# Optimization experiments

Measured on AMD Instinct MI355X. Metric: run time of the kernel, lower is better.

## Reference

```python
import jax, jax.numpy as jnp
import numpy as np

B, D, H, W, C = 2, 128, 128, 128, 4
OD, OH, OW = 96, 96, 96
RANK = 3


def setup_inputs() -> dict:
    key = jax.random.key(0)
    k1, k2 = jax.random.split(key)
    inputs = jax.random.normal(k1, (B, D, H, W, C), dtype=jnp.float32)
    # continuous sample coords in [0, size-1] per spatial dim
    scale = jnp.array([D - 1, H - 1, W - 1], dtype=jnp.float32)
    sample_coords = jax.random.uniform(k2, (B, OD, OH, OW, RANK), dtype=jnp.float32) * scale
    return {"inputs": inputs, "sample_coords": sample_coords}


def _pyramid_combination(samples, w_0, w_1):
    # recursive weighted blend over 2^rank corner samples (matches TF module)
    if len(w_0) == 1:
        return samples[0] * w_1[0] + samples[1] * w_0[0]
    f_0 = _pyramid_combination(samples[::2], w_0[:-1], w_1[:-1])
    f_1 = _pyramid_combination(samples[1::2], w_0[:-1], w_1[:-1])
    return f_0 * w_1[-1] + f_1 * w_0[-1]


def reference(inputs, sample_coords):
    # inputs: [B, D, H, W, C]; sample_coords: [B, od, oh, ow, 3]
    in_spatial = inputs.shape[1:-1]
    rank = len(in_spatial)
    batch = inputs.shape[0]

    coords = [sample_coords[..., d] for d in range(rank)]          # each [B, od, oh, ow]
    base = [jnp.floor(c) for c in coords]
    # ZERO boundary -> replicate clamp of integer coords
    floor_i = [jnp.clip(b.astype(jnp.int32), 0, in_spatial[d] - 1) for d, b in enumerate(base)]
    ceil_i = [jnp.clip((b + 1.0).astype(jnp.int32), 0, in_spatial[d] - 1) for d, b in enumerate(base)]

    # ZERO-boundary weights use the CLAMPED corner coords (faithful to source)
    w_0 = [(c - f.astype(jnp.float32))[..., None] for c, f in zip(coords, floor_i)]
    w_1 = [(ce.astype(jnp.float32) - c)[..., None] for c, ce in zip(coords, ceil_i)]

    bids = jnp.arange(batch)[:, None, None, None]                  # broadcast batch ids
    sc = (floor_i, ceil_i)

    samples = []
    for i in range(2 ** rank):
        bits = [(i >> (rank - 1 - d)) & 1 for d in range(rank)]    # dim-0 is most significant bit
        idx = [sc[bits[d]][d] for d in range(rank)]
        samples.append(inputs[bids, idx[0], idx[1], idx[2]])       # [B, od, oh, ow, C]

    return _pyramid_combination(samples, w_0, w_1)
```

## Files before the change

### kernel.cpp

```cpp
#include <hip/hip_runtime.h>


constexpr int D = 128, H = 128, W = 128;
constexpr int OD = 96, OH = 96, OW = 96;
constexpr int VOX_PER_B = OD * OH * OW;
constexpr int NVOX = 2 * VOX_PER_B;

constexpr int NBINS = 1024;
constexpr int NB1 = 216;
constexpr int SPB = 8192;
constexpr int GATHER_THREADS = 1024;
constexpr int TILE_ELEMS = 9 * 5 * 128;

constexpr size_t OFF_MATRIX  = 0;
constexpr size_t OFF_NCNT    = (size_t)NB1 * NBINS * 4;
constexpr size_t OFF_BASE    = OFF_NCNT + NBINS * 4;
constexpr size_t OFF_RECORDS = OFF_BASE + NBINS * 4;
constexpr size_t WS_REQUIRED = OFF_RECORDS + (size_t)NVOX * 16;

__device__ __forceinline__ int bin_of(float cz, float cy, int b) {
    int z0 = min(max((int)floorf(cz), 0), D - 1);
    int y0 = min(max((int)floorf(cy), 0), H - 1);
    return (((b << 4) | (z0 >> 3)) << 5) | (y0 >> 2);
}

__device__ __forceinline__ float4 f4_fma(float w, float4 a, float4 acc) {
    acc.x = fmaf(w, a.x, acc.x);
    acc.y = fmaf(w, a.y, acc.y);
    acc.z = fmaf(w, a.z, acc.z);
    acc.w = fmaf(w, a.w, acc.w);
    return acc;
}
__device__ __forceinline__ float4 f4_scale(float w, float4 a) {
    return make_float4(w * a.x, w * a.y, w * a.z, w * a.w);
}

__global__ __launch_bounds__(1024) void hist_kernel(const float* __restrict__ coords,
                                                    unsigned* __restrict__ matrix) {
    __shared__ unsigned cnt[NBINS];
    const int t = threadIdx.x;
    cnt[t] = 0;
    __syncthreads();
    const int s0 = blockIdx.x * SPB;
#pragma unroll
    for (int j = 0; j < 8; j++) {
        const int s = s0 + j * 1024 + t;
        const float cz = coords[s * 3 + 0];
        const float cy = coords[s * 3 + 1];
        const int b = (s >= VOX_PER_B) ? 1 : 0;
        atomicAdd(&cnt[bin_of(cz, cy, b)], 1u);
    }
    __syncthreads();
    matrix[blockIdx.x * NBINS + t] = cnt[t];
}

__global__ __launch_bounds__(256) void scanA_kernel(unsigned* __restrict__ matrix,
                                                    unsigned* __restrict__ ncnt) {
    const int k = blockIdx.x;
    const int t = threadIdx.x;
    const unsigned v = (t < NB1) ? matrix[t * NBINS + k] : 0u;
    __shared__ unsigned s[256];
    s[t] = v;
    __syncthreads();
    for (int off = 1; off < 256; off <<= 1) {
        unsigned u = (t >= off) ? s[t - off] : 0u;
        __syncthreads();
        s[t] += u;
        __syncthreads();
    }
    if (t < NB1) matrix[t * NBINS + k] = s[t] - v;
    if (t == 255) ncnt[k] = s[255];
}

__global__ __launch_bounds__(1024) void scanB_kernel(const unsigned* __restrict__ ncnt,
                                                     unsigned* __restrict__ base) {
    const int t = threadIdx.x;
    const unsigned v = ncnt[t];
    __shared__ unsigned s[NBINS];
    s[t] = v;
    __syncthreads();
    for (int off = 1; off < NBINS; off <<= 1) {
        unsigned u = (t >= off) ? s[t - off] : 0u;
        __syncthreads();
        s[t] += u;
        __syncthreads();
    }
    base[t] = s[t] - v;
}

__global__ __launch_bounds__(1024) void scatter_kernel(const float* __restrict__ coords,
                                                       const unsigned* __restrict__ matrix,
                                                       const unsigned* __restrict__ base,
                                                       float4* __restrict__ records) {
    __shared__ float4 rec[SPB];
    __shared__ unsigned short binid[SPB];
    __shared__ unsigned cnt[NBINS];
    __shared__ unsigned pref[NBINS];
    __shared__ unsigned gb[NBINS];
    const int t = threadIdx.x;
    const int blk = blockIdx.x;
    cnt[t] = 0;
    gb[t] = base[t] + matrix[blk * NBINS + t];
    __syncthreads();

    const int s0 = blk * SPB;
    float czr[8], cyr[8], cxr[8];
    unsigned rankr[8];
#pragma unroll
    for (int j = 0; j < 8; j++) {
        const int s = s0 + j * 1024 + t;
        czr[j] = coords[s * 3 + 0];
        cyr[j] = coords[s * 3 + 1];
        cxr[j] = coords[s * 3 + 2];
        const int b = (s >= VOX_PER_B) ? 1 : 0;
        rankr[j] = atomicAdd(&cnt[bin_of(czr[j], cyr[j], b)], 1u);
    }
    __syncthreads();

    pref[t] = cnt[t];
    __syncthreads();
    for (int off = 1; off < NBINS; off <<= 1) {
        unsigned u = (t >= off) ? pref[t - off] : 0u;
        __syncthreads();
        pref[t] += u;
        __syncthreads();
    }
    {
        unsigned ex = pref[t] - cnt[t];
        __syncthreads();
        pref[t] = ex;
    }
    __syncthreads();

#pragma unroll
    for (int j = 0; j < 8; j++) {
        const int s = s0 + j * 1024 + t;
        const int b = (s >= VOX_PER_B) ? 1 : 0;
        const int k = bin_of(czr[j], cyr[j], b);
        const unsigned slot = pref[k] + rankr[j];
        rec[slot] = make_float4(czr[j], cyr[j], cxr[j], __uint_as_float((unsigned)s));
        binid[slot] = (unsigned short)k;
    }
    __syncthreads();

#pragma unroll
    for (int j = 0; j < 8; j++) {
        const int i = j * 1024 + t;
        const int k = binid[i];
        records[gb[k] + (unsigned)(i - (int)pref[k])] = rec[i];
    }
}

__global__ __launch_bounds__(GATHER_THREADS) void gather_kernel(
    const float* __restrict__ inp,
    const float4* __restrict__ records,
    const unsigned* __restrict__ base,
    const unsigned* __restrict__ ncnt,
    float4* __restrict__ out)
{
    __shared__ float4 tile[TILE_ELEMS];
    const int k = ((blockIdx.x & 7) << 7) | (blockIdx.x >> 3);
    const int b  = k >> 9;
    const int zb = (k >> 5) & 15;
    const int yb = k & 31;
    const int t = threadIdx.x;

    const float4* bp = (const float4*)inp + ((size_t)b << 21);
    const int zlim = min(9, D - zb * 8);
    const int ylim = min(5, H - yb * 4);
    for (int i = t; i < TILE_ELEMS; i += GATHER_THREADS) {
        const int z = i / 640;
        const int r = i - z * 640;
        const int y = r >> 7;
        const int x = r & 127;
        if (z < zlim && y < ylim)
            tile[i] = bp[((zb * 8 + z) << 14) | ((yb * 4 + y) << 7) | x];
    }
    __syncthreads();

    const unsigned s = base[k];
    const unsigned n = ncnt[k];
    const int zoff = zb * 8, yoff = yb * 4;
    for (unsigned i = s + t; i < s + n; i += GATHER_THREADS) {
        const float4 r = records[i];
        const float cz = r.x, cy = r.y, cx = r.z;
        const unsigned idx = __float_as_uint(r.w);

        const int fz = (int)floorf(cz);
        const int fy = (int)floorf(cy);
        const int fx = (int)floorf(cx);
        const int z1 = min(max(fz + 1, 0), D - 1);
        const int y1 = min(max(fy + 1, 0), H - 1);
        const int x1 = min(max(fx + 1, 0), W - 1);
        const int z0 = min(max(fz, 0), D - 1);
        const int y0 = min(max(fy, 0), H - 1);
        const int x0 = min(max(fx, 0), W - 1);

        const float wz0 = (float)z1 - cz, wz1 = cz - (float)z0;
        const float wy0 = (float)y1 - cy, wy1 = cy - (float)y0;
        const float wx0 = (float)x1 - cx, wx1 = cx - (float)x0;

        const int lz0 = (z0 - zoff) * 640, lz1 = (z1 - zoff) * 640;
        const int ly0 = (y0 - yoff) * 128, ly1 = (y1 - yoff) * 128;

        const float4 s000 = tile[lz0 + ly0 + x0];
        const float4 s001 = tile[lz0 + ly0 + x1];
        const float4 s010 = tile[lz0 + ly1 + x0];
        const float4 s011 = tile[lz0 + ly1 + x1];
        const float4 s100 = tile[lz1 + ly0 + x0];
        const float4 s101 = tile[lz1 + ly0 + x1];
        const float4 s110 = tile[lz1 + ly1 + x0];
        const float4 s111 = tile[lz1 + ly1 + x1];

        float4 c00 = f4_fma(wx1, s001, f4_scale(wx0, s000));
        float4 c01 = f4_fma(wx1, s011, f4_scale(wx0, s010));
        float4 c10 = f4_fma(wx1, s101, f4_scale(wx0, s100));
        float4 c11 = f4_fma(wx1, s111, f4_scale(wx0, s110));
        float4 c0 = f4_fma(wy1, c01, f4_scale(wy0, c00));
        float4 c1 = f4_fma(wy1, c11, f4_scale(wy0, c10));
        out[idx] = f4_fma(wz1, c1, f4_scale(wz0, c0));
    }
}

__global__ __launch_bounds__(256) void direct_kernel(const float* __restrict__ inp,
                                                     const float* __restrict__ coords,
                                                     float4* __restrict__ out) {
    const int idx = blockIdx.x * 256 + threadIdx.x;
    if (idx >= NVOX) return;
    const float cz = coords[idx * 3 + 0];
    const float cy = coords[idx * 3 + 1];
    const float cx = coords[idx * 3 + 2];
    const int b = (idx >= VOX_PER_B) ? 1 : 0;

    const int fz = (int)floorf(cz);
    const int fy = (int)floorf(cy);
    const int fx = (int)floorf(cx);
    const int z1 = min(max(fz + 1, 0), D - 1);
    const int y1 = min(max(fy + 1, 0), H - 1);
    const int x1 = min(max(fx + 1, 0), W - 1);
    const int z0 = min(max(fz, 0), D - 1);
    const int y0 = min(max(fy, 0), H - 1);
    const int x0 = min(max(fx, 0), W - 1);
    const float wz0 = (float)z1 - cz, wz1 = cz - (float)z0;
    const float wy0 = (float)y1 - cy, wy1 = cy - (float)y0;
    const float wx0 = (float)x1 - cx, wx1 = cx - (float)x0;
    const float4* bp = (const float4*)inp + ((size_t)b << 21);
    const int z0o = z0 << 14, z1o = z1 << 14;
    const int y0o = y0 << 7,  y1o = y1 << 7;
    const float4 s000 = bp[z0o | y0o | x0];
    const float4 s001 = bp[z0o | y0o | x1];
    const float4 s010 = bp[z0o | y1o | x0];
    const float4 s011 = bp[z0o | y1o | x1];
    const float4 s100 = bp[z1o | y0o | x0];
    const float4 s101 = bp[z1o | y0o | x1];
    const float4 s110 = bp[z1o | y1o | x0];
    const float4 s111 = bp[z1o | y1o | x1];
    float4 c00 = f4_fma(wx1, s001, f4_scale(wx0, s000));
    float4 c01 = f4_fma(wx1, s011, f4_scale(wx0, s010));
    float4 c10 = f4_fma(wx1, s101, f4_scale(wx0, s100));
    float4 c11 = f4_fma(wx1, s111, f4_scale(wx0, s110));
    float4 c0 = f4_fma(wy1, c01, f4_scale(wy0, c00));
    float4 c1 = f4_fma(wy1, c11, f4_scale(wy0, c10));
    out[idx] = f4_fma(wz1, c1, f4_scale(wz0, c0));
}

extern "C" void kernel_launch(void* const* d_in, const int* in_sizes, int n_in,
                              void* d_out, int out_size, void* d_ws, size_t ws_size,
                              hipStream_t stream) {
    const float* inp    = (const float*)d_in[0];
    const float* coords = (const float*)d_in[1];
    float4* out = (float4*)d_out;

    if (ws_size < WS_REQUIRED) {
        direct_kernel<<<(NVOX + 255) / 256, 256, 0, stream>>>(inp, coords, out);
        return;
    }

    char* ws = (char*)d_ws;
    unsigned* matrix  = (unsigned*)(ws + OFF_MATRIX);
    unsigned* ncnt    = (unsigned*)(ws + OFF_NCNT);
    unsigned* base    = (unsigned*)(ws + OFF_BASE);
    float4*   records = (float4*)(ws + OFF_RECORDS);

    hist_kernel   <<<NB1, 1024, 0, stream>>>(coords, matrix);
    scanA_kernel  <<<NBINS, 256, 0, stream>>>(matrix, ncnt);
    scanB_kernel  <<<1, NBINS, 0, stream>>>(ncnt, base);
    scatter_kernel<<<NB1, 1024, 0, stream>>>(coords, matrix, base, records);
    gather_kernel <<<NBINS, GATHER_THREADS, 0, stream>>>(inp, records, base, ncnt, out);
}
```

Before: 174.5 us.

## Split bins along x, halve gather tiles, pack histogram counts to 16-bit

Adds an x split to the binning (2048 bins instead of 1024), so each gather block stages a 9x5x65 tile, roughly half the previous LDS footprint, and runs with 512 threads. The smaller tile is meant to allow more resident blocks per CU and more overlap between tile loads and gathers. The per-block histogram matrix is stored as packed 16-bit counts to cut workspace traffic, and scatter recomputes bin ids instead of keeping a shared binid array. The cost is more tile halo redundancy along x, more bin-index arithmetic, and a 16-bit limit on the per-block counts.

```diff
diff --git a/kernel.cpp b/kernel.cpp
--- a/kernel.cpp
+++ b/kernel.cpp
@@ -6,22 +6,23 @@
 constexpr int VOX_PER_B = OD * OH * OW;
 constexpr int NVOX = 2 * VOX_PER_B;
 
-constexpr int NBINS = 1024;
+constexpr int NBINS = 2048;
 constexpr int NB1 = 216;
 constexpr int SPB = 8192;
-constexpr int GATHER_THREADS = 1024;
-constexpr int TILE_ELEMS = 9 * 5 * 128;
+constexpr int GT = 512;
+constexpr int TILE_ELEMS = 9 * 5 * 65;
 
 constexpr size_t OFF_MATRIX  = 0;
-constexpr size_t OFF_NCNT    = (size_t)NB1 * NBINS * 4;
+constexpr size_t OFF_NCNT    = 884736;
 constexpr size_t OFF_BASE    = OFF_NCNT + NBINS * 4;
 constexpr size_t OFF_RECORDS = OFF_BASE + NBINS * 4;
 constexpr size_t WS_REQUIRED = OFF_RECORDS + (size_t)NVOX * 16;
 
-__device__ __forceinline__ int bin_of(float cz, float cy, int b) {
+__device__ __forceinline__ int bin_of(float cz, float cy, float cx, int b) {
     int z0 = min(max((int)floorf(cz), 0), D - 1);
     int y0 = min(max((int)floorf(cy), 0), H - 1);
-    return (((b << 4) | (z0 >> 3)) << 5) | (y0 >> 2);
+    int x0 = min(max((int)floorf(cx), 0), W - 1);
+    return (b << 10) | ((z0 >> 3) << 6) | ((y0 >> 2) << 1) | (x0 >> 6);
 }
 
 __device__ __forceinline__ float4 f4_fma(float w, float4 a, float4 acc) {
@@ -36,10 +37,11 @@
 }
 
 __global__ __launch_bounds__(1024) void hist_kernel(const float* __restrict__ coords,
-                                                    unsigned* __restrict__ matrix) {
+                                                    unsigned* __restrict__ matrix32) {
     __shared__ unsigned cnt[NBINS];
     const int t = threadIdx.x;
     cnt[t] = 0;
+    cnt[t + 1024] = 0;
     __syncthreads();
     const int s0 = blockIdx.x * SPB;
 #pragma unroll
@@ -47,18 +49,19 @@
         const int s = s0 + j * 1024 + t;
         const float cz = coords[s * 3 + 0];
         const float cy = coords[s * 3 + 1];
+        const float cx = coords[s * 3 + 2];
         const int b = (s >= VOX_PER_B) ? 1 : 0;
-        atomicAdd(&cnt[bin_of(cz, cy, b)], 1u);
-    }
-    __syncthreads();
-    matrix[blockIdx.x * NBINS + t] = cnt[t];
-}
-
-__global__ __launch_bounds__(256) void scanA_kernel(unsigned* __restrict__ matrix,
+        atomicAdd(&cnt[bin_of(cz, cy, cx, b)], 1u);
+    }
+    __syncthreads();
+    matrix32[blockIdx.x * 1024 + t] = cnt[2 * t] | (cnt[2 * t + 1] << 16);
+}
+
+__global__ __launch_bounds__(256) void scanA_kernel(unsigned short* __restrict__ matrix16,
                                                     unsigned* __restrict__ ncnt) {
     const int k = blockIdx.x;
     const int t = threadIdx.x;
-    const unsigned v = (t < NB1) ? matrix[t * NBINS + k] : 0u;
+    const unsigned v = (t < NB1) ? (unsigned)matrix16[t * NBINS + k] : 0u;
     __shared__ unsigned s[256];
     s[t] = v;
     __syncthreads();
@@ -68,39 +71,41 @@
         s[t] += u;
         __syncthreads();
     }
-    if (t < NB1) matrix[t * NBINS + k] = s[t] - v;
+    if (t < NB1) matrix16[t * NBINS + k] = (unsigned short)(s[t] - v);
     if (t == 255) ncnt[k] = s[255];
 }
 
 __global__ __launch_bounds__(1024) void scanB_kernel(const unsigned* __restrict__ ncnt,
                                                      unsigned* __restrict__ base) {
     const int t = threadIdx.x;
-    const unsigned v = ncnt[t];
-    __shared__ unsigned s[NBINS];
-    s[t] = v;
-    __syncthreads();
-    for (int off = 1; off < NBINS; off <<= 1) {
+    const unsigned c0 = ncnt[2 * t];
+    const unsigned c1 = ncnt[2 * t + 1];
+    __shared__ unsigned s[1024];
+    s[t] = c0 + c1;
+    __syncthreads();
+    for (int off = 1; off < 1024; off <<= 1) {
         unsigned u = (t >= off) ? s[t - off] : 0u;
         __syncthreads();
         s[t] += u;
         __syncthreads();
     }
-    base[t] = s[t] - v;
+    const unsigned ex = s[t] - (c0 + c1);
+    base[2 * t] = ex;
+    base[2 * t + 1] = ex + c0;
 }
 
 __global__ __launch_bounds__(1024) void scatter_kernel(const float* __restrict__ coords,
-                                                       const unsigned* __restrict__ matrix,
+                                                       const unsigned* __restrict__ matrix32,
                                                        const unsigned* __restrict__ base,
                                                        float4* __restrict__ records) {
     __shared__ float4 rec[SPB];
-    __shared__ unsigned short binid[SPB];
-    __shared__ unsigned cnt[NBINS];
+    __shared__ unsigned cntgb[NBINS];
     __shared__ unsigned pref[NBINS];
-    __shared__ unsigned gb[NBINS];
+    __shared__ unsigned s[1024];
     const int t = threadIdx.x;
     const int blk = blockIdx.x;
-    cnt[t] = 0;
-    gb[t] = base[t] + matrix[blk * NBINS + t];
+    cntgb[2 * t] = 0;
+    cntgb[2 * t + 1] = 0;
     __syncthreads();
 
     const int s0 = blk * SPB;
@@ -108,50 +113,56 @@
     unsigned rankr[8];
 #pragma unroll
     for (int j = 0; j < 8; j++) {
-        const int s = s0 + j * 1024 + t;
-        czr[j] = coords[s * 3 + 0];
-        cyr[j] = coords[s * 3 + 1];
-        cxr[j] = coords[s * 3 + 2];
-        const int b = (s >= VOX_PER_B) ? 1 : 0;
-        rankr[j] = atomicAdd(&cnt[bin_of(czr[j], cyr[j], b)], 1u);
-    }
-    __syncthreads();
-
-    pref[t] = cnt[t];
-    __syncthreads();
-    for (int off = 1; off < NBINS; off <<= 1) {
-        unsigned u = (t >= off) ? pref[t - off] : 0u;
-        __syncthreads();
-        pref[t] += u;
-        __syncthreads();
-    }
-    {
-        unsigned ex = pref[t] - cnt[t];
-        __syncthreads();
-        pref[t] = ex;
-    }
+        const int smp = s0 + j * 1024 + t;
+        czr[j] = coords[smp * 3 + 0];
+        cyr[j] = coords[smp * 3 + 1];
+        cxr[j] = coords[smp * 3 + 2];
+        const int b = (smp >= VOX_PER_B) ? 1 : 0;
+        rankr[j] = atomicAdd(&cntgb[bin_of(czr[j], cyr[j], cxr[j], b)], 1u);
+    }
+    __syncthreads();
+
+    const unsigned c0 = cntgb[2 * t];
+    const unsigned c1 = cntgb[2 * t + 1];
+    s[t] = c0 + c1;
+    __syncthreads();
+    for (int off = 1; off < 1024; off <<= 1) {
+        unsigned u = (t >= off) ? s[t - off] : 0u;
+        __syncthreads();
+        s[t] += u;
+        __syncthreads();
+    }
+    const unsigned ex = s[t] - (c0 + c1);
+    pref[2 * t] = ex;
+    pref[2 * t + 1] = ex + c0;
     __syncthreads();
 
 #pragma unroll
     for (int j = 0; j < 8; j++) {
-        const int s = s0 + j * 1024 + t;
-        const int b = (s >= VOX_PER_B) ? 1 : 0;
-        const int k = bin_of(czr[j], cyr[j], b);
-        const unsigned slot = pref[k] + rankr[j];
-        rec[slot] = make_float4(czr[j], cyr[j], cxr[j], __uint_as_float((unsigned)s));
-        binid[slot] = (unsigned short)k;
-    }
+        const int smp = s0 + j * 1024 + t;
+        const int b = (smp >= VOX_PER_B) ? 1 : 0;
+        const int k = bin_of(czr[j], cyr[j], cxr[j], b);
+        rec[pref[k] + rankr[j]] =
+            make_float4(czr[j], cyr[j], cxr[j], __uint_as_float((unsigned)smp));
+    }
+
+    const unsigned m = matrix32[blk * 1024 + t];
+    cntgb[2 * t]     = base[2 * t]     + (m & 0xFFFFu);
+    cntgb[2 * t + 1] = base[2 * t + 1] + (m >> 16);
     __syncthreads();
 
 #pragma unroll
     for (int j = 0; j < 8; j++) {
         const int i = j * 1024 + t;
-        const int k = binid[i];
-        records[gb[k] + (unsigned)(i - (int)pref[k])] = rec[i];
-    }
-}
-
-__global__ __launch_bounds__(GATHER_THREADS) void gather_kernel(
+        const float4 r = rec[i];
+        const unsigned idx = __float_as_uint(r.w);
+        const int b = (idx >= (unsigned)VOX_PER_B) ? 1 : 0;
+        const int k = bin_of(r.x, r.y, r.z, b);
+        records[cntgb[k] + (unsigned)(i - (int)pref[k])] = r;
+    }
+}
+
+__global__ __launch_bounds__(GT) void gather_kernel(
     const float* __restrict__ inp,
     const float4* __restrict__ records,
     const unsigned* __restrict__ base,
@@ -159,29 +170,32 @@
     float4* __restrict__ out)
 {
     __shared__ float4 tile[TILE_ELEMS];
-    const int k = ((blockIdx.x & 7) << 7) | (blockIdx.x >> 3);
-    const int b  = k >> 9;
-    const int zb = (k >> 5) & 15;
-    const int yb = k & 31;
+    const int k = ((blockIdx.x & 7) << 8) | (blockIdx.x >> 3);
+    const int b  = k >> 10;
+    const int zb = (k >> 6) & 15;
+    const int yb = (k >> 1) & 31;
+    const int xb = k & 1;
     const int t = threadIdx.x;
 
     const float4* bp = (const float4*)inp + ((size_t)b << 21);
     const int zlim = min(9, D - zb * 8);
     const int ylim = min(5, H - yb * 4);
-    for (int i = t; i < TILE_ELEMS; i += GATHER_THREADS) {
-        const int z = i / 640;
-        const int r = i - z * 640;
-        const int y = r >> 7;
-        const int x = r & 127;
-        if (z < zlim && y < ylim)
-            tile[i] = bp[((zb * 8 + z) << 14) | ((yb * 4 + y) << 7) | x];
-    }
-    __syncthreads();
-
-    const unsigned s = base[k];
+    for (int i = t; i < TILE_ELEMS; i += GT) {
+        const int z = i / 325;
+        const int r = i - z * 325;
+        const int y = r / 65;
+        const int x = r - y * 65;
+        if (z < zlim && y < ylim) {
+            const int gx = min(xb * 64 + x, W - 1);
+            tile[i] = bp[((zb * 8 + z) << 14) | ((yb * 4 + y) << 7) | gx];
+        }
+    }
+    __syncthreads();
+
+    const unsigned st = base[k];
     const unsigned n = ncnt[k];
-    const int zoff = zb * 8, yoff = yb * 4;
-    for (unsigned i = s + t; i < s + n; i += GATHER_THREADS) {
+    const int zoff = zb * 8, yoff = yb * 4, xoff = xb * 64;
+    for (unsigned i = st + t; i < st + n; i += GT) {
         const float4 r = records[i];
         const float cz = r.x, cy = r.y, cx = r.z;
         const unsigned idx = __float_as_uint(r.w);
@@ -200,17 +214,18 @@
         const float wy0 = (float)y1 - cy, wy1 = cy - (float)y0;
         const float wx0 = (float)x1 - cx, wx1 = cx - (float)x0;
 
-        const int lz0 = (z0 - zoff) * 640, lz1 = (z1 - zoff) * 640;
-        const int ly0 = (y0 - yoff) * 128, ly1 = (y1 - yoff) * 128;
-
-        const float4 s000 = tile[lz0 + ly0 + x0];
-        const float4 s001 = tile[lz0 + ly0 + x1];
-        const float4 s010 = tile[lz0 + ly1 + x0];
-        const float4 s011 = tile[lz0 + ly1 + x1];
-        const float4 s100 = tile[lz1 + ly0 + x0];
-        const float4 s101 = tile[lz1 + ly0 + x1];
-        const float4 s110 = tile[lz1 + ly1 + x0];
-        const float4 s111 = tile[lz1 + ly1 + x1];
+        const int lz0 = (z0 - zoff) * 325, lz1 = (z1 - zoff) * 325;
+        const int ly0 = (y0 - yoff) * 65,  ly1 = (y1 - yoff) * 65;
+        const int lx0 = x0 - xoff,         lx1 = x1 - xoff;
+
+        const float4 s000 = tile[lz0 + ly0 + lx0];
+        const float4 s001 = tile[lz0 + ly0 + lx1];
+        const float4 s010 = tile[lz0 + ly1 + lx0];
+        const float4 s011 = tile[lz0 + ly1 + lx1];
+        const float4 s100 = tile[lz1 + ly0 + lx0];
+        const float4 s101 = tile[lz1 + ly0 + lx1];
+        const float4 s110 = tile[lz1 + ly1 + lx0];
+        const float4 s111 = tile[lz1 + ly1 + lx1];
 
         float4 c00 = f4_fma(wx1, s001, f4_scale(wx0, s000));
         float4 c01 = f4_fma(wx1, s011, f4_scale(wx0, s010));
@@ -277,14 +292,15 @@
     }
 
     char* ws = (char*)d_ws;
-    unsigned* matrix  = (unsigned*)(ws + OFF_MATRIX);
-    unsigned* ncnt    = (unsigned*)(ws + OFF_NCNT);
-    unsigned* base    = (unsigned*)(ws + OFF_BASE);
-    float4*   records = (float4*)(ws + OFF_RECORDS);
-
-    hist_kernel   <<<NB1, 1024, 0, stream>>>(coords, matrix);
-    scanA_kernel  <<<NBINS, 256, 0, stream>>>(matrix, ncnt);
-    scanB_kernel  <<<1, NBINS, 0, stream>>>(ncnt, base);
-    scatter_kernel<<<NB1, 1024, 0, stream>>>(coords, matrix, base, records);
-    gather_kernel <<<NBINS, GATHER_THREADS, 0, stream>>>(inp, records, base, ncnt, out);
-}
+    unsigned*       matrix32 = (unsigned*)(ws + OFF_MATRIX);
+    unsigned short* matrix16 = (unsigned short*)(ws + OFF_MATRIX);
+    unsigned*       ncnt     = (unsigned*)(ws + OFF_NCNT);
+    unsigned*       base     = (unsigned*)(ws + OFF_BASE);
+    float4*         records  = (float4*)(ws + OFF_RECORDS);
+
+    hist_kernel   <<<NB1, 1024, 0, stream>>>(coords, matrix32);
+    scanA_kernel  <<<NBINS, 256, 0, stream>>>(matrix16, ncnt);
+    scanB_kernel  <<<1, 1024, 0, stream>>>(ncnt, base);
+    scatter_kernel<<<NB1, 1024, 0, stream>>>(coords, matrix32, base, records);
+    gather_kernel <<<NBINS, GT, 0, stream>>>(inp, records, base, ncnt, out);
+}
```

After: 177.2 us. Within noise of the previous version (+1.6%).
